# Performance work log

Hardware: AMD Instinct MI355X
Metric: run time of the kernel (lower is better)

The kernel has to match this reference:

```python
import jax, jax.numpy as jnp
import numpy as np

LEVELS = 16
FEATURES = 2
HASHMAP_SIZE = 524288  # 2**19
BASE_RES = 16
PER_LEVEL_SCALE = 1.5
N_POINTS = 2097152  # 2**21

# Per-level grid resolutions, computed exactly like the torch code: int(base*scale**l)
_RES = np.array([int(BASE_RES * PER_LEVEL_SCALE ** l) for l in range(LEVELS)], dtype=np.float32)

# Instant-NGP spatial hash primes
_P1, _P2, _P3 = np.int32(73856093), np.int32(19349663), np.int32(83492791)


def setup_inputs() -> dict:
    key = jax.random.key(0)
    k1, k2 = jax.random.split(key)
    x = jax.random.uniform(k1, (N_POINTS, 3), dtype=jnp.float32)
    # Stacked learned hash tables: [L, T, F], init randn*0.01 as in the module
    tables = jax.random.normal(k2, (LEVELS, HASHMAP_SIZE, FEATURES), dtype=jnp.float32) * 0.01
    return {"x": x, "tables": tables}


def reference(x, tables):
    # x: [N, 3] float; tables: [L, T, F] float
    res = jnp.asarray(_RES)                       # [L]
    pos = x[None, :, :] * res[:, None, None]      # [L, N, 3]
    p = jnp.floor(pos).astype(jnp.int32)          # [L, N, 3] (matches torch .int())
    # Spatial hash with int32 wrap-around, identical to torch int32 semantics
    h = (p[..., 0] * _P1) ^ (p[..., 1] * _P2) ^ (p[..., 2] * _P3)
    idx = jnp.mod(h, np.int32(HASHMAP_SIZE))      # [L, N], nonnegative (sign of divisor)
    emb = jax.vmap(lambda t, i: t[i])(tables, idx)  # [L, N, F] per-level gather
    n = x.shape[0]
    # concat over levels along last dim -> [N, L*F]
    return jnp.transpose(emb, (1, 0, 2)).reshape(n, LEVELS * FEATURES)
```

## Files before the change

### kernel.cpp

```cpp
#include <hip/hip_runtime.h>

#define LEVELS 16
#define TSIZE 524288
#define TMASK (TSIZE - 1)
#define TPB 256
#define GPPT 8
#define CHUNK (TPB * GPPT)

typedef float f2v __attribute__((ext_vector_type(2)));
typedef float f4v __attribute__((ext_vector_type(4)));

__device__ __constant__ float c_res[LEVELS] = {
    16.f, 24.f, 36.f, 54.f, 81.f, 121.f, 182.f, 273.f,
    410.f, 615.f, 922.f, 1383.f, 2075.f, 3113.f, 4670.f, 7006.f
};

__device__ __forceinline__ unsigned hash_idx(float px, float py, float pz, float r)
{
    const int ix = (int)floorf(px * r);
    const int iy = (int)floorf(py * r);
    const int iz = (int)floorf(pz * r);
    const unsigned h = (unsigned)ix * 73856093u
                     ^ (unsigned)iy * 19349663u
                     ^ (unsigned)iz * 83492791u;
    return h & TMASK;
}



__global__ __launch_bounds__(TPB) void hash_kernel(
    const float* __restrict__ x,
    unsigned* __restrict__ idxw,
    int n)
{
    __shared__ float xs[CHUNK * 3];
    const int c = blockIdx.x;
    const int t = threadIdx.x;
    const long long base = (long long)c * CHUNK;
    unsigned* __restrict__ islab = idxw + (size_t)c * LEVELS * CHUNK;

    if (base + CHUNK <= n) {
        const f4v* __restrict__ xg = reinterpret_cast<const f4v*>(x + 3 * base);
#pragma unroll
        for (int j = 0; j < 6; ++j) {
            const int s = j * TPB + t;
            *reinterpret_cast<f4v*>(&xs[4 * s]) = xg[s];
        }
        __syncthreads();

#pragma unroll
        for (int j = 0; j < GPPT; ++j) {
            const int local = j * TPB + t;
            const float px = xs[3 * local + 0];
            const float py = xs[3 * local + 1];
            const float pz = xs[3 * local + 2];
#pragma unroll
            for (int l = 0; l < LEVELS; ++l) {
                const unsigned id = hash_idx(px, py, pz, c_res[l]);
                __builtin_nontemporal_store(id, islab + l * CHUNK + local);
            }
        }
    } else {
        for (int j = 0; j < GPPT; ++j) {
            const int local = j * TPB + t;
            const long long p = base + local;
            if (p < n) {
                const float px = x[3 * p + 0];
                const float py = x[3 * p + 1];
                const float pz = x[3 * p + 2];
                for (int l = 0; l < LEVELS; ++l)
                    islab[l * CHUNK + local] = hash_idx(px, py, pz, c_res[l]);
            }
        }
    }
}

__global__ __launch_bounds__(TPB) void gather_kernel(
    const unsigned* __restrict__ idxr,
    const float* __restrict__ tables,
    f2v* __restrict__ ws,
    int n, int bpl)
{
    const int b = blockIdx.x;
    const int half = b / (8 * bpl);
    const int r = b % (8 * bpl);
    const int level = half * 8 + (r & 7);
    const int c = r >> 3;
    const int t = threadIdx.x;

    const float* __restrict__ tbl = tables + (size_t)level * (TSIZE * 2);
    f2v* __restrict__ slab = ws + ((size_t)c * LEVELS + level) * CHUNK;
    const unsigned* __restrict__ islab = idxr + ((size_t)c * LEVELS + level) * CHUNK;
    const long long base = (long long)c * CHUNK;

    if (base + CHUNK <= n) {
        unsigned idx[GPPT];
#pragma unroll
        for (int j = 0; j < GPPT; ++j)
            idx[j] = islab[j * TPB + t];

        f2v e[GPPT];
#pragma unroll
        for (int j = 0; j < GPPT; ++j)
            e[j] = *reinterpret_cast<const f2v*>(tbl + 2 * (size_t)idx[j]);

#pragma unroll
        for (int j = 0; j < GPPT; ++j)
            __builtin_nontemporal_store(e[j], slab + j * TPB + t);
    } else {
        for (int j = 0; j < GPPT; ++j) {
            const int local = j * TPB + t;
            if (base + local < n) {
                const unsigned id = islab[local];
                const f2v e = *reinterpret_cast<const f2v*>(tbl + 2 * (size_t)id);
                __builtin_nontemporal_store(e, slab + local);
            }
        }
    }
}

__global__ __launch_bounds__(TPB) void gather_x_kernel(
    const float* __restrict__ x,
    const float* __restrict__ tables,
    f2v* __restrict__ ws,
    int n, int bpl)
{
    const int b = blockIdx.x;
    const int half = b / (8 * bpl);
    const int r = b % (8 * bpl);
    const int level = half * 8 + (r & 7);
    const int c = r >> 3;
    const int t = threadIdx.x;

    const float rs = c_res[level];
    const float* __restrict__ tbl = tables + (size_t)level * (TSIZE * 2);
    f2v* __restrict__ slab = ws + ((size_t)c * LEVELS + level) * CHUNK;
    const long long base = (long long)c * CHUNK;

    if (base + CHUNK <= n) {
        const float* __restrict__ xb = x + 3 * base;
        float px[GPPT], py[GPPT], pz[GPPT];
#pragma unroll
        for (int j = 0; j < GPPT; ++j) {
            const int local = j * TPB + t;
            px[j] = xb[3 * local + 0];
            py[j] = xb[3 * local + 1];
            pz[j] = xb[3 * local + 2];
        }
        unsigned idx[GPPT];
#pragma unroll
        for (int j = 0; j < GPPT; ++j)
            idx[j] = hash_idx(px[j], py[j], pz[j], rs);
        f2v e[GPPT];
#pragma unroll
        for (int j = 0; j < GPPT; ++j)
            e[j] = *reinterpret_cast<const f2v*>(tbl + 2 * (size_t)idx[j]);
#pragma unroll
        for (int j = 0; j < GPPT; ++j)
            __builtin_nontemporal_store(e[j], slab + j * TPB + t);
    } else {
#pragma unroll
        for (int j = 0; j < GPPT; ++j) {
            const int local = j * TPB + t;
            const long long p = base + local;
            if (p < n) {
                const float qx = x[3 * p + 0];
                const float qy = x[3 * p + 1];
                const float qz = x[3 * p + 2];
                const unsigned idx = hash_idx(qx, qy, qz, rs);
                const f2v e = *reinterpret_cast<const f2v*>(tbl + 2 * (size_t)idx);
                __builtin_nontemporal_store(e, slab + local);
            }
        }
    }
}

__global__ __launch_bounds__(TPB) void assemble_kernel(
    const f2v* __restrict__ ws,
    float* __restrict__ out,
    int n)
{
    const int c = blockIdx.x;
    const int t = threadIdx.x;
    const int q = t & 7;
    const int sub = t >> 3;

    const f2v* __restrict__ wa = ws + ((size_t)c * LEVELS + 2 * q) * CHUNK;
    const f2v* __restrict__ wb = wa + CHUNK;
    const long long base = (long long)c * CHUNK;

    if (base + CHUNK <= n) {
#pragma unroll 8
        for (int u = 0; u < CHUNK / 64; ++u) {
            const int lp = 2 * (u * 32 + sub);
            const f4v a = __builtin_nontemporal_load(
                reinterpret_cast<const f4v*>(wa + lp));
            const f4v b = __builtin_nontemporal_load(
                reinterpret_cast<const f4v*>(wb + lp));
            f4v v0, v1;
            v0.x = a.x; v0.y = a.y; v0.z = b.x; v0.w = b.y;
            v1.x = a.z; v1.y = a.w; v1.z = b.z; v1.w = b.w;
            float* row = out + (size_t)(base + lp) * (2 * LEVELS) + 4 * q;
            __builtin_nontemporal_store(v0, reinterpret_cast<f4v*>(row));
            __builtin_nontemporal_store(v1, reinterpret_cast<f4v*>(row + 2 * LEVELS));
        }
    } else {
#pragma unroll 8
        for (int u = 0; u < CHUNK / 32; ++u) {
            const int lp = u * 32 + sub;
            const long long pt = base + lp;
            if (pt < n) {
                const f2v a = __builtin_nontemporal_load(wa + lp);
                const f2v b = __builtin_nontemporal_load(wb + lp);
                f4v v;
                v.x = a.x; v.y = a.y; v.z = b.x; v.w = b.y;
                __builtin_nontemporal_store(
                    v, reinterpret_cast<f4v*>(out + (size_t)pt * (2 * LEVELS) + 4 * q));
            }
        }
    }
}

#define ROWW 34
__global__ __launch_bounds__(TPB) void hashgrid_fused(
    const float* __restrict__ x,
    const float* __restrict__ tables,
    float* __restrict__ out,
    int n)
{
    __shared__ float lds[TPB * ROWW];
    const int t = threadIdx.x;

    for (long long base = (long long)blockIdx.x * TPB; base < n;
         base += (long long)gridDim.x * TPB) {
        const int p = (int)base + t;
        float px = 0.f, py = 0.f, pz = 0.f;
        if (p < n) {
            px = x[3 * (size_t)p + 0];
            py = x[3 * (size_t)p + 1];
            pz = x[3 * (size_t)p + 2];
        }
#pragma unroll
        for (int l = 0; l < LEVELS; ++l) {
            if (p < n) {
                const unsigned idx = hash_idx(px, py, pz, c_res[l]);
                const f2v e = *reinterpret_cast<const f2v*>(
                    tables + (((size_t)l * TSIZE + idx) << 1));
                *reinterpret_cast<f2v*>(lds + t * ROWW + 2 * l) = e;
            }
            __syncthreads();
        }
#pragma unroll
        for (int it = 0; it < 8; ++it) {
            const int lp = it * 32 + (t >> 3);
            const int qq = t & 7;
            const int gp = (int)base + lp;
            if (gp < n) {
                const f2v a = *reinterpret_cast<const f2v*>(lds + lp * ROWW + 4 * qq);
                const f2v b = *reinterpret_cast<const f2v*>(lds + lp * ROWW + 4 * qq + 2);
                f4v v;
                v.x = a.x; v.y = a.y; v.z = b.x; v.w = b.y;
                __builtin_nontemporal_store(
                    v, reinterpret_cast<f4v*>(out + (size_t)gp * (2 * LEVELS) + 4 * qq));
            }
        }
        __syncthreads();
    }
}

extern "C" void kernel_launch(void* const* d_in, const int* in_sizes, int n_in,
                              void* d_out, int out_size, void* d_ws, size_t ws_size,
                              hipStream_t stream)
{
    const float* x      = (const float*)d_in[0];
    const float* tables = (const float*)d_in[1];
    float* out          = (float*)d_out;
    const int n = in_sizes[0] / 3;

    const int bpl = (n + CHUNK - 1) / CHUNK;
    const size_t slab_bytes = (size_t)bpl * LEVELS * CHUNK * sizeof(f2v);
    const size_t idx_bytes  = (size_t)bpl * LEVELS * CHUNK * sizeof(unsigned);

    if (ws_size < slab_bytes) {
        int grid = 1024;
        const int nblocks = (n + TPB - 1) / TPB;
        if (nblocks < grid) grid = nblocks;
        hashgrid_fused<<<grid, TPB, 0, stream>>>(x, tables, out, n);
        return;
    }

    f2v* ws = (f2v*)d_ws;

    if (ws_size >= slab_bytes + idx_bytes) {
        unsigned* idxw = (unsigned*)((char*)d_ws + slab_bytes);
        hash_kernel<<<bpl, TPB, 0, stream>>>(x, idxw, n);
        gather_kernel<<<2 * 8 * bpl, TPB, 0, stream>>>(idxw, tables, ws, n, bpl);
    } else {
        gather_x_kernel<<<2 * 8 * bpl, TPB, 0, stream>>>(x, tables, ws, n, bpl);
    }
    assemble_kernel<<<bpl, TPB, 0, stream>>>(ws, out, n);
}
```

Baseline: 351.4 us.

## Serve coarse levels from dense LDS-resident tables and rebalance gather block mapping

Adds a remap kernel that builds dense per-cell feature tables for the two coarsest levels (16^3 and 24^3 cells), which are small enough to sit in LDS. The hash kernel writes dense linear indices for those levels, and a new gather_lo kernel serves them from shared memory instead of doing random global gathers into 4MB hash tables. The remaining 14 levels use the existing gather kernel with a new block-to-work mapping spread across 8 interleaved groups. The cost is an extra kernel launch and the remap pass. Hash stores also switch from nontemporal to normal stores. Any point coordinate equal to 1.0 would index past the dense range, which is an edge-case risk.

```diff
diff --git a/kernel.cpp b/kernel.cpp
--- a/kernel.cpp
+++ b/kernel.cpp
@@ -7,6 +7,11 @@
 #define GPPT 8
 #define CHUNK (TPB * GPPT)
 
+#define C0 4096
+#define C1 13824
+#define C1H 6912
+#define GLO 4
+
 typedef float f2v __attribute__((ext_vector_type(2)));
 typedef float f4v __attribute__((ext_vector_type(4)));
 
@@ -15,23 +20,41 @@
     410.f, 615.f, 922.f, 1383.f, 2075.f, 3113.f, 4670.f, 7006.f
 };
 
+__device__ __forceinline__ unsigned hash_iii(int ix, int iy, int iz)
+{
+    return ((unsigned)ix * 73856093u
+          ^ (unsigned)iy * 19349663u
+          ^ (unsigned)iz * 83492791u) & TMASK;
+}
+
 __device__ __forceinline__ unsigned hash_idx(float px, float py, float pz, float r)
 {
-    const int ix = (int)floorf(px * r);
-    const int iy = (int)floorf(py * r);
-    const int iz = (int)floorf(pz * r);
-    const unsigned h = (unsigned)ix * 73856093u
-                     ^ (unsigned)iy * 19349663u
-                     ^ (unsigned)iz * 83492791u;
-    return h & TMASK;
-}
-
-
+    return hash_iii((int)floorf(px * r), (int)floorf(py * r), (int)floorf(pz * r));
+}
+
+
+
+__global__ __launch_bounds__(TPB) void remap_kernel(
+    const float* __restrict__ tables,
+    f2v* __restrict__ dense)
+{
+    const int e = blockIdx.x * TPB + threadIdx.x;
+    if (e >= C0 + C1) return;
+    int id, r, lvl;
+    if (e < C0) { lvl = 0; r = 16; id = e; }
+    else        { lvl = 1; r = 24; id = e - C0; }
+    int ix, iy, iz;
+    if (r == 16) { ix = id & 15; iy = (id >> 4) & 15; iz = id >> 8; }
+    else         { ix = id % 24; iy = (id / 24) % 24; iz = id / 576; }
+    const unsigned h = hash_iii(ix, iy, iz);
+    const float* __restrict__ tbl = tables + (size_t)lvl * (TSIZE * 2);
+    dense[e] = *reinterpret_cast<const f2v*>(tbl + 2 * (size_t)h);
+}
 
 __global__ __launch_bounds__(TPB) void hash_kernel(
     const float* __restrict__ x,
     unsigned* __restrict__ idxw,
-    int n)
+    int n, int lo_dense)
 {
     __shared__ float xs[CHUNK * 3];
     const int c = blockIdx.x;
@@ -56,8 +79,18 @@
             const float pz = xs[3 * local + 2];
 #pragma unroll
             for (int l = 0; l < LEVELS; ++l) {
-                const unsigned id = hash_idx(px, py, pz, c_res[l]);
-                __builtin_nontemporal_store(id, islab + l * CHUNK + local);
+                const float rs = c_res[l];
+                const int ix = (int)floorf(px * rs);
+                const int iy = (int)floorf(py * rs);
+                const int iz = (int)floorf(pz * rs);
+                unsigned id;
+                if (lo_dense && l < 2) {
+                    const int ri = (l == 0) ? 16 : 24;
+                    id = (unsigned)(ix + ri * (iy + ri * iz));
+                } else {
+                    id = hash_iii(ix, iy, iz);
+                }
+                islab[l * CHUNK + local] = id;
             }
         }
     } else {
@@ -68,8 +101,113 @@
                 const float px = x[3 * p + 0];
                 const float py = x[3 * p + 1];
                 const float pz = x[3 * p + 2];
-                for (int l = 0; l < LEVELS; ++l)
-                    islab[l * CHUNK + local] = hash_idx(px, py, pz, c_res[l]);
+                for (int l = 0; l < LEVELS; ++l) {
+                    const float rs = c_res[l];
+                    const int ix = (int)floorf(px * rs);
+                    const int iy = (int)floorf(py * rs);
+                    const int iz = (int)floorf(pz * rs);
+                    unsigned id;
+                    if (lo_dense && l < 2) {
+                        const int ri = (l == 0) ? 16 : 24;
+                        id = (unsigned)(ix + ri * (iy + ri * iz));
+                    } else {
+                        id = hash_iii(ix, iy, iz);
+                    }
+                    islab[l * CHUNK + local] = id;
+                }
+            }
+        }
+    }
+}
+
+__global__ __launch_bounds__(TPB) void gather_lo(
+    const unsigned* __restrict__ idxr,
+    const f2v* __restrict__ dense,
+    f2v* __restrict__ ws,
+    int n, int bpl, int nb)
+{
+    __shared__ f2v dlds[C1H];
+    const int b = blockIdx.x;
+    const int t = threadIdx.x;
+    const int lvl = (b < nb) ? 0 : 1;
+    const int cbase = (lvl ? (b - nb) : b) * GLO;
+
+    if (lvl == 0) {
+        const f4v* __restrict__ d0 = reinterpret_cast<const f4v*>(dense);
+        f4v* __restrict__ dst = reinterpret_cast<f4v*>(dlds);
+#pragma unroll
+        for (int s = 0; s < C0 / 2 / TPB; ++s)
+            dst[s * TPB + t] = d0[s * TPB + t];
+        __syncthreads();
+
+        for (int cc = 0; cc < GLO; ++cc) {
+            const int c = cbase + cc;
+            if (c >= bpl) break;
+            const long long base = (long long)c * CHUNK;
+            const unsigned* __restrict__ islab = idxr + ((size_t)c * LEVELS + 0) * CHUNK;
+            f2v* __restrict__ slab = ws + ((size_t)c * LEVELS + 0) * CHUNK;
+            if (base + CHUNK <= n) {
+                unsigned idx[GPPT];
+#pragma unroll
+                for (int j = 0; j < GPPT; ++j)
+                    idx[j] = islab[j * TPB + t];
+                f2v e[GPPT];
+#pragma unroll
+                for (int j = 0; j < GPPT; ++j)
+                    e[j] = dlds[idx[j]];
+#pragma unroll
+                for (int j = 0; j < GPPT; ++j)
+                    __builtin_nontemporal_store(e[j], slab + j * TPB + t);
+            } else {
+                for (int j = 0; j < GPPT; ++j) {
+                    const int local = j * TPB + t;
+                    if (base + local < n)
+                        slab[local] = dlds[islab[local]];
+                }
+            }
+        }
+    } else {
+        unsigned I[GLO][GPPT];
+        for (int cc = 0; cc < GLO; ++cc) {
+            const int c = cbase + cc;
+            const unsigned* __restrict__ islab =
+                idxr + ((size_t)c * LEVELS + 1) * CHUNK;
+            for (int j = 0; j < GPPT; ++j) {
+                const int local = j * TPB + t;
+                const long long p = (long long)c * CHUNK + local;
+                I[cc][j] = (c < bpl && p < n) ? islab[local] : 0xFFFFFFFFu;
+            }
+        }
+        f2v E[GLO][GPPT];
+
+        for (int s = t; s < C1H; s += TPB) dlds[s] = dense[C0 + s];
+        __syncthreads();
+        for (int cc = 0; cc < GLO; ++cc)
+            for (int j = 0; j < GPPT; ++j)
+                if (I[cc][j] < C1H) E[cc][j] = dlds[I[cc][j]];
+        __syncthreads();
+
+        for (int s = t; s < C1H; s += TPB) dlds[s] = dense[C0 + C1H + s];
+        __syncthreads();
+        for (int cc = 0; cc < GLO; ++cc)
+            for (int j = 0; j < GPPT; ++j)
+                if (I[cc][j] >= C1H && I[cc][j] < C1)
+                    E[cc][j] = dlds[I[cc][j] - C1H];
+
+        for (int cc = 0; cc < GLO; ++cc) {
+            const int c = cbase + cc;
+            if (c >= bpl) break;
+            const long long base = (long long)c * CHUNK;
+            f2v* __restrict__ slab = ws + ((size_t)c * LEVELS + 1) * CHUNK;
+            if (base + CHUNK <= n) {
+#pragma unroll
+                for (int j = 0; j < GPPT; ++j)
+                    __builtin_nontemporal_store(E[cc][j], slab + j * TPB + t);
+            } else {
+                for (int j = 0; j < GPPT; ++j) {
+                    const int local = j * TPB + t;
+                    if (base + local < n) slab[local] = E[cc][j];
+                }
             }
         }
     }
@@ -79,13 +217,16 @@
     const unsigned* __restrict__ idxr,
     const float* __restrict__ tables,
     f2v* __restrict__ ws,
-    int n, int bpl)
-{
-    const int b = blockIdx.x;
-    const int half = b / (8 * bpl);
-    const int r = b % (8 * bpl);
-    const int level = half * 8 + (r & 7);
-    const int c = r >> 3;
+    int n, int bpl, int lvl_start, int nlv)
+{
+    const long long total = (long long)nlv * bpl;
+    const int k = blockIdx.x & 7;
+    const long long s = blockIdx.x >> 3;
+    const long long w = ((total * k) >> 3) + s;
+    if (w >= ((total * (k + 1)) >> 3)) return;
+    const int lrel = (int)(w / bpl);
+    const int level = lvl_start + lrel;
+    const int c = (int)(w - (long long)lrel * bpl);
     const int t = threadIdx.x;
 
     const float* __restrict__ tbl = tables + (size_t)level * (TSIZE * 2);
@@ -278,8 +419,9 @@
     const int n = in_sizes[0] / 3;
 
     const int bpl = (n + CHUNK - 1) / CHUNK;
-    const size_t slab_bytes = (size_t)bpl * LEVELS * CHUNK * sizeof(f2v);
-    const size_t idx_bytes  = (size_t)bpl * LEVELS * CHUNK * sizeof(unsigned);
+    const size_t slab_bytes  = (size_t)bpl * LEVELS * CHUNK * sizeof(f2v);
+    const size_t idx_bytes   = (size_t)bpl * LEVELS * CHUNK * sizeof(unsigned);
+    const size_t dense_bytes = (size_t)(C0 + C1) * sizeof(f2v);
 
     if (ws_size < slab_bytes) {
         int grid = 1024;
@@ -291,10 +433,23 @@
 
     f2v* ws = (f2v*)d_ws;
 
-    if (ws_size >= slab_bytes + idx_bytes) {
+    if (ws_size >= slab_bytes + idx_bytes + dense_bytes) {
         unsigned* idxw = (unsigned*)((char*)d_ws + slab_bytes);
-        hash_kernel<<<bpl, TPB, 0, stream>>>(x, idxw, n);
-        gather_kernel<<<2 * 8 * bpl, TPB, 0, stream>>>(idxw, tables, ws, n, bpl);
+        f2v* dense = (f2v*)((char*)d_ws + slab_bytes + idx_bytes);
+        const int nb = (bpl + GLO - 1) / GLO;
+        const long long total_hi = 14LL * bpl;
+
+        remap_kernel<<<(C0 + C1 + TPB - 1) / TPB, TPB, 0, stream>>>(tables, dense);
+        hash_kernel<<<bpl, TPB, 0, stream>>>(x, idxw, n, 1);
+        gather_lo<<<2 * nb, TPB, 0, stream>>>(idxw, dense, ws, n, bpl, nb);
+        gather_kernel<<<(int)(8 * ((total_hi + 7) / 8)), TPB, 0, stream>>>(
+            idxw, tables, ws, n, bpl, 2, 14);
+    } else if (ws_size >= slab_bytes + idx_bytes) {
+        unsigned* idxw = (unsigned*)((char*)d_ws + slab_bytes);
+        const long long total = 16LL * bpl;
+        hash_kernel<<<bpl, TPB, 0, stream>>>(x, idxw, n, 0);
+        gather_kernel<<<(int)(8 * ((total + 7) / 8)), TPB, 0, stream>>>(
+            idxw, tables, ws, n, bpl, 0, 16);
     } else {
         gather_x_kernel<<<2 * 8 * bpl, TPB, 0, stream>>>(x, tables, ws, n, bpl);
     }
```

Result: faster. 330.6 us (-5.9%).
